# Performance work log

Measured on AMD Instinct MI355X. Metric: run time of the kernel, lower is better.

The kernel has to match this reference:

```python
import jax, jax.numpy as jnp
import numpy as np

HIDDEN = 512
BATCH = 128
SEQ = 512


def setup_inputs() -> dict:
    key = jax.random.key(0)
    k_ins, k_res, k1, k2, k3, k4 = jax.random.split(key, 6)
    bound = 1.0 / np.sqrt(HIDDEN)  # torch GRUCell default init
    u = lambda k, shape: jax.random.uniform(k, shape, jnp.float32, -bound, bound)
    return {
        "hidden": jnp.zeros((BATCH, HIDDEN), jnp.float32),
        "ins": jax.random.normal(k_ins, (BATCH, SEQ, HIDDEN), jnp.float32),
        "resets": jax.random.randint(k_res, (BATCH, SEQ), 0, 2).astype(jnp.bool_),
        "W_ih": u(k1, (3 * HIDDEN, HIDDEN)),
        "W_hh": u(k2, (3 * HIDDEN, HIDDEN)),
        "b_ih": u(k3, (3 * HIDDEN,)),
        "b_hh": u(k4, (3 * HIDDEN,)),
    }


def reference(hidden, ins, resets, W_ih, W_hh, b_ih, b_hh):
    # PyTorch GRUCell gate order: reset, update, new
    def step(h, xt):
        x, rmask = xt  # x: [B,H], rmask: [B]
        h = jnp.where(rmask[:, None], jnp.zeros_like(h), h)  # reset carry
        gi = x @ W_ih.T + b_ih   # [B, 3H]
        gh = h @ W_hh.T + b_hh   # [B, 3H]
        i_r, i_z, i_n = jnp.split(gi, 3, axis=-1)
        h_r, h_z, h_n = jnp.split(gh, 3, axis=-1)
        r = jax.nn.sigmoid(i_r + h_r)
        z = jax.nn.sigmoid(i_z + h_z)
        n = jnp.tanh(i_n + r * h_n)
        h_new = (1.0 - z) * n + z * h
        return h_new, h_new

    xs = (jnp.swapaxes(ins, 0, 1), jnp.swapaxes(resets, 0, 1))  # time-major
    h_final, ys = jax.lax.scan(step, hidden, xs)
    return h_final, jnp.swapaxes(ys, 0, 1)  # outputs back to [B,T,H]
```

## Files before the change

kernel.cpp:

```cpp
#include <hip/hip_runtime.h>
#include <hip/hip_bf16.h>
#include <stdint.h>

#define T_SEQ 512
#define HID   512
#define BATCH 128
#define G_B   8
#define G_N   32
#define BB    (BATCH / G_B)
#define HC    (HID / G_N)
#define NROW  (3 * HC)
#define HFIN  (BATCH * HID)
#define WSTR  512
#define XSTR  520
#define GSTR  20

using f32x4  = __attribute__((ext_vector_type(4))) float;
using short8 = __attribute__((ext_vector_type(8))) short;
using bfs4   = __attribute__((ext_vector_type(4))) short;

typedef const __attribute__((address_space(1))) void* gas_t;
typedef __attribute__((address_space(3))) void* las_t;

__device__ __forceinline__ short8 pack8(float a0, float a1, float a2, float a3,
                                        float a4, float a5, float a6, float a7) {
    union { uint32_t u[4]; short8 s; } r;
    asm("v_cvt_pk_bf16_f32 %0, %1, %2" : "=v"(r.u[0]) : "v"(a0), "v"(a1));
    asm("v_cvt_pk_bf16_f32 %0, %1, %2" : "=v"(r.u[1]) : "v"(a2), "v"(a3));
    asm("v_cvt_pk_bf16_f32 %0, %1, %2" : "=v"(r.u[2]) : "v"(a4), "v"(a5));
    asm("v_cvt_pk_bf16_f32 %0, %1, %2" : "=v"(r.u[3]) : "v"(a6), "v"(a7));
    return r.s;
}

__device__ __forceinline__ uint16_t f2bf(float f) {
    uint32_t u = __builtin_bit_cast(uint32_t, f);
    return (uint16_t)((u + 0x7fffu + ((u >> 16) & 1u)) >> 16);
}

__device__ __forceinline__ int lws(int row, int ko) {
    return row * WSTR + (ko ^ ((row & 7) << 3));
}

__global__ void __launch_bounds__(128, 1) gru_scan(
    const float* __restrict__ hidden,
    const float* __restrict__ ins,
    const int*   __restrict__ resets,
    const float* __restrict__ W_ih,
    const float* __restrict__ W_hh,
    const float* __restrict__ b_ih,
    const float* __restrict__ b_hh,
    float* __restrict__ out,
    uint32_t* __restrict__ flags,
    unsigned short* __restrict__ xbs)
{
    __shared__ __align__(16) short ldsW[2][NROW * WSTR];
    __shared__ __align__(16) float ldsX[BB * XSTR];
    __shared__ __align__(16) float giB[64 * GSTR];
    __shared__ __align__(16) float hnvB[64 * 4];

    const int wg   = blockIdx.x;
    const int bb   = wg & 7;
    const int nn   = wg >> 3;
    const int tid  = threadIdx.x;
    const int lane = tid & 63;
    const int wv   = tid >> 6;
    const int l15  = lane & 15;
    const int lg   = lane >> 4;

#define STAGE_X(T_) do {                                                      \
        _Pragma("unroll")                                                     \
        for (int i_ = 0; i_ < 32; ++i_) {                                     \
            const int r_ = i_ >> 1, hf_ = i_ & 1;                             \
            const float* src_ = ins + ((size_t)(bb * BB + r_) * T_SEQ + (T_)) \
                                   * HID + hf_ * 256 + lane * 4;              \
            float* dst_ = (float*)&ldsX[r_ * XSTR + hf_ * 256];               \
            __builtin_amdgcn_global_load_lds((gas_t)src_, (las_t)dst_,        \
                                             16, 0, 0);                       \
        }                                                                     \
    } while (0)

    if (wv) STAGE_X(0);

    for (int idx = tid; idx < NROW * (HID / 4); idx += 128) {
        const int row = idx >> 7;
        const int k4  = (idx & 127) << 2;
        const int g   = row >> 4;
        const int i   = row & 15;
        const int grow = g * HID + nn * HC + i;
        f32x4 wi = *(const f32x4*)&W_ih[(size_t)grow * HID + k4];
        f32x4 wh = *(const f32x4*)&W_hh[(size_t)grow * HID + k4];
        bfs4 si = { (short)f2bf(wi[0]), (short)f2bf(wi[1]), (short)f2bf(wi[2]), (short)f2bf(wi[3]) };
        bfs4 sh = { (short)f2bf(wh[0]), (short)f2bf(wh[1]), (short)f2bf(wh[2]), (short)f2bf(wh[3]) };
        *(bfs4*)&ldsW[0][lws(row, k4)] = si;
        *(bfs4*)&ldsW[1][lws(row, k4)] = sh;
    }
    __syncthreads();

    const int arow  = bb * BB + l15;
    const int drow0 = bb * BB + lg * 4;
    const int dcol  = nn * HC + l15;
    float* const ys = out + HFIN;

    if (wv) {
        for (int t = 0; t < T_SEQ; ++t) {
            asm volatile("s_waitcnt vmcnt(0)" ::: "memory");
            __builtin_amdgcn_sched_barrier(0);

            short8 af[16];
            const float* xr = &ldsX[l15 * XSTR + lg * 8];
            #pragma unroll
            for (int kt = 0; kt < 16; ++kt) {
                f32x4 x0 = *(const f32x4*)(xr + kt * 32);
                f32x4 x1 = *(const f32x4*)(xr + kt * 32 + 4);
                af[kt] = pack8(x0[0], x0[1], x0[2], x0[3], x1[0], x1[1], x1[2], x1[3]);
            }

            f32x4 aIr = {0,0,0,0}, aIz = {0,0,0,0}, aIn = {0,0,0,0};
            #pragma unroll
            for (int kt = 0; kt < 16; ++kt) {
                const int ko = kt * 32 + lg * 8;
                aIr = __builtin_amdgcn_mfma_f32_16x16x32_bf16(af[kt], *(const short8*)&ldsW[0][lws(l15, ko)], aIr, 0, 0, 0);
                aIz = __builtin_amdgcn_mfma_f32_16x16x32_bf16(af[kt], *(const short8*)&ldsW[0][lws(16 + l15, ko)], aIz, 0, 0, 0);
                aIn = __builtin_amdgcn_mfma_f32_16x16x32_bf16(af[kt], *(const short8*)&ldsW[0][lws(32 + l15, ko)], aIn, 0, 0, 0);
            }
            *(f32x4*)&giB[lane * GSTR + 0] = aIr;
            *(f32x4*)&giB[lane * GSTR + 4] = aIz;
            *(f32x4*)&giB[lane * GSTR + 8] = aIn;
            asm volatile("s_waitcnt lgkmcnt(0)" ::: "memory");
            __builtin_amdgcn_s_barrier();
            if (t + 1 < T_SEQ) STAGE_X(t + 1);
            __builtin_amdgcn_s_barrier();

            f32x4 hn = *(const f32x4*)&hnvB[lane * 4];
            #pragma unroll
            for (int j = 0; j < 4; ++j) {
                const int r_ = drow0 + j;
                ys[((size_t)r_ * T_SEQ + t) * HID + dcol] = hn[j];
                if (t == T_SEQ - 1) out[(size_t)r_ * HID + dcol] = hn[j];
            }
        }
    } else {
        const float bir = b_ih[dcol], biz = b_ih[HID + dcol], bin_ = b_ih[2 * HID + dcol];
        const float bhr = b_hh[dcol], bhz = b_hh[HID + dcol], bhn  = b_hh[2 * HID + dcol];

        float hprev[4];
        #pragma unroll
        for (int j = 0; j < 4; ++j)
            hprev[j] = hidden[(size_t)(drow0 + j) * HID + dcol];

        const uint32_t* fp = flags + bb * 32 + (lane & 31);
        uint32_t* const fme = flags + bb * 32 + nn;

        for (int t = 0; t < T_SEQ; ++t) {
            short8 ah[16];
            int rstA, rstD[4];
            rstA = resets[(size_t)arow * T_SEQ + t];
            #pragma unroll
            for (int j = 0; j < 4; ++j)
                rstD[j] = resets[(size_t)(drow0 + j) * T_SEQ + t];

            if (t == 0) {
                const float* hrow = hidden + (size_t)arow * HID + lg * 8;
                const float am = rstA ? 0.f : 1.f;
                #pragma unroll
                for (int kt = 0; kt < 16; ++kt) {
                    f32x4 h0 = *(const f32x4*)(hrow + kt * 32);
                    f32x4 h1 = *(const f32x4*)(hrow + kt * 32 + 4);
                    ah[kt] = pack8(am * h0[0], am * h0[1], am * h0[2], am * h0[3],
                                   am * h1[0], am * h1[1], am * h1[2], am * h1[3]);
                }
            } else {
                uint32_t f;
                do {
                    asm volatile("global_load_dword %0, %1, off sc0 sc1\n\t"
                                 "s_waitcnt vmcnt(0)"
                                 : "=v"(f) : "v"(fp) : "memory");
                } while (!__all((int)(f >= (uint32_t)t)));
                __builtin_amdgcn_sched_barrier(0);

                const unsigned short* hb = xbs + (size_t)((t - 1) & 1) * HFIN
                                               + (size_t)arow * HID + lg * 8;
#define LOADH(K, OFFS) \
    asm volatile("global_load_dwordx4 %0, %1, off offset:" OFFS " sc0 sc1" \
                 : "=v"(ah[K]) : "v"(hb) : "memory")
                LOADH(0, "0");    LOADH(1, "64");   LOADH(2, "128");  LOADH(3, "192");
                LOADH(4, "256");  LOADH(5, "320");  LOADH(6, "384");  LOADH(7, "448");
                LOADH(8, "512");  LOADH(9, "576");  LOADH(10, "640"); LOADH(11, "704");
                LOADH(12, "768"); LOADH(13, "832"); LOADH(14, "896"); LOADH(15, "960");
#undef LOADH
                asm volatile("s_waitcnt vmcnt(0)" ::: "memory");
                __builtin_amdgcn_sched_barrier(0);
                if (rstA) {
                    const short8 z8 = {0,0,0,0,0,0,0,0};
                    #pragma unroll
                    for (int kt = 0; kt < 16; ++kt) ah[kt] = z8;
                }
            }

            __builtin_amdgcn_s_barrier();

            f32x4 aIr = *(const f32x4*)&giB[lane * GSTR + 0];
            f32x4 aIz = *(const f32x4*)&giB[lane * GSTR + 4];
            f32x4 aIn = *(const f32x4*)&giB[lane * GSTR + 8];

            f32x4 aHr = {0,0,0,0}, aHz = {0,0,0,0}, aHn = {0,0,0,0};
            #pragma unroll
            for (int kt = 0; kt < 16; ++kt) {
                const int ko = kt * 32 + lg * 8;
                aHr = __builtin_amdgcn_mfma_f32_16x16x32_bf16(ah[kt], *(const short8*)&ldsW[1][lws(l15, ko)], aHr, 0, 0, 0);
                aHz = __builtin_amdgcn_mfma_f32_16x16x32_bf16(ah[kt], *(const short8*)&ldsW[1][lws(16 + l15, ko)], aHz, 0, 0, 0);
                aHn = __builtin_amdgcn_mfma_f32_16x16x32_bf16(ah[kt], *(const short8*)&ldsW[1][lws(32 + l15, ko)], aHn, 0, 0, 0);
            }

            f32x4 hv;
            #pragma unroll
            for (int j = 0; j < 4; ++j) {
                const float hp = rstD[j] ? 0.f : hprev[j];
                const float gr = aIr[j] + bir + aHr[j] + bhr;
                const float rg = 1.f / (1.f + __expf(-gr));
                const float gz = aIz[j] + biz + aHz[j] + bhz;
                const float zg = 1.f / (1.f + __expf(-gz));
                float gn = aIn[j] + bin_ + rg * (aHn[j] + bhn);
                gn = fminf(fmaxf(gn, -15.f), 15.f);
                const float e2 = __expf(2.f * gn);
                const float ng = (e2 - 1.f) / (e2 + 1.f);
                const float hn = (1.f - zg) * ng + zg * hp;
                hprev[j] = hn;
                hv[j] = hn;
            }
            *(f32x4*)&hnvB[lane * 4] = hv;

            if (t < T_SEQ - 1) {
                #pragma unroll
                for (int j = 0; j < 4; ++j) {
                    uint32_t v = f2bf(hv[j]);
                    unsigned short* p = xbs + (size_t)(t & 1) * HFIN
                                            + (size_t)(drow0 + j) * HID + dcol;
                    asm volatile("global_store_short %0, %1, off sc0 sc1"
                                 :: "v"(p), "v"(v) : "memory");
                }
                asm volatile("s_waitcnt vmcnt(0)" ::: "memory");
                if (lane == 0) {
                    uint32_t tag = (uint32_t)(t + 1);
                    asm volatile("global_store_dword %0, %1, off sc0 sc1"
                                 :: "v"(fme), "v"(tag) : "memory");
                }
            }
            asm volatile("s_waitcnt lgkmcnt(0)" ::: "memory");
            __builtin_amdgcn_s_barrier();
        }
    }
#undef STAGE_X
}

extern "C" void kernel_launch(void* const* d_in, const int* in_sizes, int n_in,
                              void* d_out, int out_size, void* d_ws, size_t ws_size,
                              hipStream_t stream) {
    const float* hidden = (const float*)d_in[0];
    const float* ins    = (const float*)d_in[1];
    const int*   resets = (const int*)d_in[2];
    const float* W_ih   = (const float*)d_in[3];
    const float* W_hh   = (const float*)d_in[4];
    const float* b_ih   = (const float*)d_in[5];
    const float* b_hh   = (const float*)d_in[6];
    float* out = (float*)d_out;
    uint32_t* flags = (uint32_t*)d_ws;
    unsigned short* xbs = (unsigned short*)((char*)d_ws + 1024);

    hipMemsetAsync(flags, 0, 1024, stream);
    gru_scan<<<dim3(G_B * G_N), dim3(128), 0, stream>>>(
        hidden, ins, resets, W_ih, W_hh, b_ih, b_hh, out, flags, xbs);
}
```

Before: 1.720 ms.

## Tighten recurrent critical path: LDS resets, register-cached W_hh, pipelined flag polling

Reset masks for the workgroup's batch rows are staged into LDS once at startup, so the per-step global reads of resets go away. Half of the W_hh fragments (first 8 k-tiles of all three gates) are preloaded into registers so the recurrent MFMA loop does fewer LDS reads on the serial path. Flag polling keeps two loads in flight so a retry does not pay a full round-trip, and the bf16 hidden stores are issued per element right after each is computed, ahead of the LDS hnv write. The cost is much higher VGPR pressure (24 short8 registers) and extra LDS for the reset table.

```diff
diff --git a/kernel.cpp b/kernel.cpp
--- a/kernel.cpp
+++ b/kernel.cpp
@@ -57,6 +57,7 @@
     __shared__ __align__(16) float ldsX[BB * XSTR];
     __shared__ __align__(16) float giB[64 * GSTR];
     __shared__ __align__(16) float hnvB[64 * 4];
+    __shared__ unsigned char ldsRb[T_SEQ * BB];
 
     const int wg   = blockIdx.x;
     const int bb   = wg & 7;
@@ -94,6 +95,12 @@
         *(bfs4*)&ldsW[0][lws(row, k4)] = si;
         *(bfs4*)&ldsW[1][lws(row, k4)] = sh;
     }
+    for (int idx = tid; idx < BB * T_SEQ; idx += 128) {
+        const int r = idx >> 9;
+        const int t = idx & (T_SEQ - 1);
+        ldsRb[t * BB + r] =
+            (unsigned char)resets[(size_t)(bb * BB + r) * T_SEQ + t];
+    }
     __syncthreads();
 
     const int arow  = bb * BB + l15;
@@ -148,17 +155,25 @@
         for (int j = 0; j < 4; ++j)
             hprev[j] = hidden[(size_t)(drow0 + j) * HID + dcol];
 
+        short8 wpre[24];
+        #pragma unroll
+        for (int g = 0; g < 3; ++g)
+            #pragma unroll
+            for (int kt = 0; kt < 8; ++kt)
+                wpre[g * 8 + kt] =
+                    *(const short8*)&ldsW[1][lws(g * 16 + l15, kt * 32 + lg * 8)];
+
         const uint32_t* fp = flags + bb * 32 + (lane & 31);
         uint32_t* const fme = flags + bb * 32 + nn;
 
         for (int t = 0; t < T_SEQ; ++t) {
+            const int rstA = ldsRb[t * BB + l15];
+            int rstD[4];
+            #pragma unroll
+            for (int j = 0; j < 4; ++j)
+                rstD[j] = ldsRb[t * BB + lg * 4 + j];
+
             short8 ah[16];
-            int rstA, rstD[4];
-            rstA = resets[(size_t)arow * T_SEQ + t];
-            #pragma unroll
-            for (int j = 0; j < 4; ++j)
-                rstD[j] = resets[(size_t)(drow0 + j) * T_SEQ + t];
-
             if (t == 0) {
                 const float* hrow = hidden + (size_t)arow * HID + lg * 8;
                 const float am = rstA ? 0.f : 1.f;
@@ -170,12 +185,20 @@
                                    am * h1[0], am * h1[1], am * h1[2], am * h1[3]);
                 }
             } else {
-                uint32_t f;
-                do {
-                    asm volatile("global_load_dword %0, %1, off sc0 sc1\n\t"
-                                 "s_waitcnt vmcnt(0)"
-                                 : "=v"(f) : "v"(fp) : "memory");
-                } while (!__all((int)(f >= (uint32_t)t)));
+                uint32_t f0, f1;
+                asm volatile("global_load_dword %0, %2, off sc0 sc1\n\t"
+                             "global_load_dword %1, %2, off sc0 sc1"
+                             : "=v"(f0), "=v"(f1) : "v"(fp) : "memory");
+                for (;;) {
+                    asm volatile("s_waitcnt vmcnt(1)" ::: "memory");
+                    if (__all((int)(f0 >= (uint32_t)t))) break;
+                    asm volatile("global_load_dword %0, %1, off sc0 sc1"
+                                 : "=v"(f0) : "v"(fp) : "memory");
+                    asm volatile("s_waitcnt vmcnt(1)" ::: "memory");
+                    if (__all((int)(f1 >= (uint32_t)t))) break;
+                    asm volatile("global_load_dword %0, %1, off sc0 sc1"
+                                 : "=v"(f1) : "v"(fp) : "memory");
+                }
                 __builtin_amdgcn_sched_barrier(0);
 
                 const unsigned short* hb = xbs + (size_t)((t - 1) & 1) * HFIN
@@ -205,7 +228,13 @@
 
             f32x4 aHr = {0,0,0,0}, aHz = {0,0,0,0}, aHn = {0,0,0,0};
             #pragma unroll
-            for (int kt = 0; kt < 16; ++kt) {
+            for (int kt = 0; kt < 8; ++kt) {
+                aHr = __builtin_amdgcn_mfma_f32_16x16x32_bf16(ah[kt], wpre[kt],      aHr, 0, 0, 0);
+                aHz = __builtin_amdgcn_mfma_f32_16x16x32_bf16(ah[kt], wpre[8 + kt],  aHz, 0, 0, 0);
+                aHn = __builtin_amdgcn_mfma_f32_16x16x32_bf16(ah[kt], wpre[16 + kt], aHn, 0, 0, 0);
+            }
+            #pragma unroll
+            for (int kt = 8; kt < 16; ++kt) {
                 const int ko = kt * 32 + lg * 8;
                 aHr = __builtin_amdgcn_mfma_f32_16x16x32_bf16(ah[kt], *(const short8*)&ldsW[1][lws(l15, ko)], aHr, 0, 0, 0);
                 aHz = __builtin_amdgcn_mfma_f32_16x16x32_bf16(ah[kt], *(const short8*)&ldsW[1][lws(16 + l15, ko)], aHz, 0, 0, 0);
@@ -227,18 +256,16 @@
                 const float hn = (1.f - zg) * ng + zg * hp;
                 hprev[j] = hn;
                 hv[j] = hn;
-            }
-            *(f32x4*)&hnvB[lane * 4] = hv;
-
-            if (t < T_SEQ - 1) {
-                #pragma unroll
-                for (int j = 0; j < 4; ++j) {
-                    uint32_t v = f2bf(hv[j]);
+                if (t < T_SEQ - 1) {
+                    uint32_t v = f2bf(hn);
                     unsigned short* p = xbs + (size_t)(t & 1) * HFIN
                                             + (size_t)(drow0 + j) * HID + dcol;
                     asm volatile("global_store_short %0, %1, off sc0 sc1"
                                  :: "v"(p), "v"(v) : "memory");
                 }
+            }
+
+            if (t < T_SEQ - 1) {
                 asm volatile("s_waitcnt vmcnt(0)" ::: "memory");
                 if (lane == 0) {
                     uint32_t tag = (uint32_t)(t + 1);
@@ -246,6 +273,8 @@
                                  :: "v"(fme), "v"(tag) : "memory");
                 }
             }
+
+            *(f32x4*)&hnvB[lane * 4] = hv;
             asm volatile("s_waitcnt lgkmcnt(0)" ::: "memory");
             __builtin_amdgcn_s_barrier();
         }
```

Result: slower. 1.841 ms (+7.1%).
